# Performance work log

Hardware: AMD Instinct MI355X
Metric: run time of the kernel (lower is better)

The kernel has to match this reference:

```python
import jax, jax.numpy as jnp
import numpy as np

B, N, M, D = 8, 1024, 2048, 1024


def setup_inputs() -> dict:
    key = jax.random.key(0)
    k1, k2, k3 = jax.random.split(key, 3)
    text_features = jax.random.normal(k1, (B, N, D), dtype=jnp.float32)
    audio_features = jax.random.normal(k2, (B, M, D), dtype=jnp.float32)
    sigma = jnp.ones((1,), dtype=jnp.float32)  # learnable bandwidth, initial_sigma=1.0
    # audio lengths in [M//4, M) so no softmax row is fully masked
    audio_lengths = jnp.maximum(
        jax.random.randint(k3, (B,), 0, M), M // 4
    ).astype(jnp.int32)
    return {
        "text_features": text_features,
        "audio_features": audio_features,
        "sigma": sigma,
        "audio_lengths": audio_lengths,
    }


def reference(text_features, audio_features, sigma, audio_lengths):
    b, n, d = text_features.shape
    m = audio_features.shape[1]
    s = jnp.abs(sigma[0]) + 1e-8

    # QK^T / sqrt(d)  -> (B, N, M)
    scores = jnp.einsum("bnd,bmd->bnm", text_features, audio_features) / jnp.sqrt(
        jnp.float32(d)
    )

    # Gaussian relative positional bias: -|i/N - j/M|^2 / (2 sigma^2)
    text_pos = jnp.arange(n, dtype=jnp.float32) / n    # (N,)
    audio_pos = jnp.arange(m, dtype=jnp.float32) / m   # (M,)
    d_rel = jnp.abs(text_pos[:, None] - audio_pos[None, :])  # (N, M)
    scores = scores - d_rel**2 / (2.0 * s * s)

    # mask padded audio positions per batch element
    valid = jnp.arange(m)[None, :] < audio_lengths[:, None]  # (B, M) bool
    scores = jnp.where(valid[:, None, :], scores, -jnp.inf)

    attention_weights = jax.nn.softmax(scores, axis=-1)  # (B, N, M)
    enhanced = jnp.einsum("bnm,bmd->bnd", attention_weights, audio_features)
    return enhanced, attention_weights
```

## Files before the change

kernel.cpp:

```cpp
#include <hip/hip_runtime.h>
#include <hip/hip_bf16.h>

#define BB 8
#define NN 1024
#define MM 2048
#define DD 1024

typedef __attribute__((ext_vector_type(8))) __bf16 bfrag8;
typedef __attribute__((ext_vector_type(4))) float ffrag4;

__device__ __forceinline__ unsigned short f2bf(float f) {
  union { float f; unsigned u; } x; x.f = f;
  unsigned r = x.u + 0x7FFFu + ((x.u >> 16) & 1u);
  return (unsigned short)(r >> 16);
}

__device__ __forceinline__ void gload_lds16(const unsigned short* g, unsigned short* l) {
  __builtin_amdgcn_global_load_lds(
      (const __attribute__((address_space(1))) void*)g,
      (__attribute__((address_space(3))) void*)l, 16, 0, 0);
}

#define SCHED0() __builtin_amdgcn_sched_barrier(0)
#define MFMA16x16x32 __builtin_amdgcn_mfma_f32_16x16x32_bf16

__device__ __forceinline__ void stage_half(const unsigned short* gbase, int ldk,
                                           unsigned short* ldst,
                                           int w, int r0, int slog) {
  const unsigned short* g = gbase + (size_t)(w * 8 + r0) * ldk + slog;
  gload_lds16(g, ldst + w * 512);
  gload_lds16(g + (size_t)64 * ldk, ldst + 4096 + w * 512);
}

#define TSTR 68
__global__ __launch_bounds__(256) void ta_prep(
    const float* __restrict__ Q, const float* __restrict__ V,
    unsigned short* __restrict__ Qbf,
    unsigned short* __restrict__ Kbf, unsigned short* __restrict__ VT,
    float* __restrict__ sums)
{
  __shared__ unsigned short Tls[64 * TSTR];
  const int bid = blockIdx.x;
  const int t = threadIdx.x;

  if (bid < 4096) {
    int tt = bid * 256 + t;
    const float4* src = reinterpret_cast<const float4*>(Q) + tt * 2;
    float4 a = src[0], b = src[1];
    ushort4 lo = { f2bf(a.x), f2bf(a.y), f2bf(a.z), f2bf(a.w) };
    ushort4 hi = { f2bf(b.x), f2bf(b.y), f2bf(b.z), f2bf(b.w) };
    ushort4* dst = reinterpret_cast<ushort4*>(Qbf) + tt * 2;
    dst[0] = lo; dst[1] = hi;
  } else if (bid < 8192) {
    const int id = bid - 4096;
    const int dt = id & 15;
    const int mt = (id >> 4) & 31;
    const int b  = id >> 9;

    const float* Vb = V + (size_t)b * MM * DD + (size_t)(mt * 64) * DD + dt * 64;
#pragma unroll
    for (int it = 0; it < 4; ++it) {
      int slot = t + 256 * it;
      int row  = slot >> 4;
      int c4   = slot & 15;
      float4 a = *reinterpret_cast<const float4*>(Vb + (size_t)row * DD + c4 * 4);
      ushort4 h = { f2bf(a.x), f2bf(a.y), f2bf(a.z), f2bf(a.w) };
      *reinterpret_cast<ushort4*>(&Tls[row * TSTR + c4 * 4]) = h;
    }
    __syncthreads();

    unsigned short* Kb = Kbf + (size_t)b * MM * DD + (size_t)(mt * 64) * DD + dt * 64;
    unsigned short* Vt = VT  + (size_t)b * DD * MM + (size_t)(dt * 64) * MM + mt * 64;
#pragma unroll
    for (int it = 0; it < 4; ++it) {
      int slot = t + 256 * it;
      int row  = slot >> 4;
      int c4   = slot & 15;
      *reinterpret_cast<ushort4*>(Kb + (size_t)row * DD + c4 * 4) =
          *reinterpret_cast<const ushort4*>(&Tls[row * TSTR + c4 * 4]);
      ushort4 tv = { Tls[(c4 * 4 + 0) * TSTR + row],
                     Tls[(c4 * 4 + 1) * TSTR + row],
                     Tls[(c4 * 4 + 2) * TSTR + row],
                     Tls[(c4 * 4 + 3) * TSTR + row] };
      *reinterpret_cast<ushort4*>(Vt + (size_t)row * MM + c4 * 4) = tv;
    }
  } else {
    int tt = (bid - 8192) * 256 + t;
    sums[tt] = 0.0f;
  }
}

__global__ void ta_zero(float* __restrict__ sums) {
  int t = blockIdx.x * 256 + threadIdx.x;
  if (t < BB * NN) sums[t] = 0.0f;
}

__global__ __launch_bounds__(512, 2) void ta_gemm1x(
    const unsigned short* __restrict__ Q,
    const unsigned short* __restrict__ K,
    const float* __restrict__ sigma,
    const int* __restrict__ lens,
    unsigned short* __restrict__ Ebf,
    float* __restrict__ rowsum)
{
  const int lin = blockIdx.x + 8 * (blockIdx.y + 4 * blockIdx.z);
  const int wid = (lin & 7) * 32 + (lin >> 3);
  const int bj = wid & 7, bi = (wid >> 3) & 3, b = wid >> 5;

  const int t = threadIdx.x;
  const int lane = t & 63, w = t >> 6;
  const int wr = w >> 2, wc = w & 3;
  __shared__ unsigned short S[73728];

  const unsigned short* Qb = Q + (size_t)b * NN * DD + (size_t)(bi * 256) * DD;
  const unsigned short* Kb = K + (size_t)b * MM * DD + (size_t)(bj * 256) * DD;

  const int r  = lane & 15, qd = lane >> 4;
  const int r0 = (lane >> 3) & 7;
  const int slog = ((lane & 7) ^ r0) << 3;
  const int cs0 = ((qd)     ^ (r & 7)) << 3;
  const int cs1 = ((4 + qd) ^ (r & 7)) << 3;

  ffrag4 acc[8][4] = {};

  {
    unsigned short* T0 = &S[0];
    stage_half(Qb,                        DD, T0,          w, r0, slog);
    stage_half(Qb + (size_t)128 * DD,     DD, T0 + 8192,   w, r0, slog);
    stage_half(Kb,                        DD, T0 + 16384,  w, r0, slog);
    stage_half(Kb + (size_t)128 * DD,     DD, T0 + 24576,  w, r0, slog);
    unsigned short* T1 = &S[32768];
    stage_half(Qb + 64,                    DD, T1,          w, r0, slog);
    stage_half(Qb + (size_t)128 * DD + 64, DD, T1 + 8192,   w, r0, slog);
    stage_half(Kb + 64,                    DD, T1 + 16384,  w, r0, slog);
    stage_half(Kb + (size_t)128 * DD + 64, DD, T1 + 24576,  w, r0, slog);
    asm volatile("s_waitcnt vmcnt(8)" ::: "memory");
    __builtin_amdgcn_s_barrier();
  }

#pragma unroll 2
  for (int kt = 0; kt < 16; ++kt) {
    const int p = kt & 1;
    unsigned short* Ab = &S[p * 32768 + wr * 8192];
    unsigned short* Bb = &S[p * 32768 + 16384 + (wc >> 1) * 8192];
    const int brb = (wc & 1) * 64;
    bfrag8 af[4][2], bf0[2][2], bf1[2][2];

#pragma unroll
    for (int mi = 0; mi < 4; ++mi) {
      const unsigned short* a = &Ab[(mi * 16 + r) * 64];
      af[mi][0] = *reinterpret_cast<const bfrag8*>(a + cs0);
      af[mi][1] = *reinterpret_cast<const bfrag8*>(a + cs1);
    }
#pragma unroll
    for (int jj = 0; jj < 2; ++jj) {
      const unsigned short* bp = &Bb[(brb + jj * 16 + r) * 64];
      bf0[jj][0] = *reinterpret_cast<const bfrag8*>(bp + cs0);
      bf0[jj][1] = *reinterpret_cast<const bfrag8*>(bp + cs1);
    }
    asm volatile("s_waitcnt lgkmcnt(0)" ::: "memory");
    SCHED0(); __builtin_amdgcn_s_setprio(1);
#pragma unroll
    for (int mi = 0; mi < 4; ++mi)
#pragma unroll
      for (int jj = 0; jj < 2; ++jj) {
        acc[mi][jj] = MFMA16x16x32(af[mi][0], bf0[jj][0], acc[mi][jj], 0, 0, 0);
        acc[mi][jj] = MFMA16x16x32(af[mi][1], bf0[jj][1], acc[mi][jj], 0, 0, 0);
      }
    __builtin_amdgcn_s_setprio(0); SCHED0();

#pragma unroll
    for (int jj = 0; jj < 2; ++jj) {
      const unsigned short* bp = &Bb[(brb + (2 + jj) * 16 + r) * 64];
      bf1[jj][0] = *reinterpret_cast<const bfrag8*>(bp + cs0);
      bf1[jj][1] = *reinterpret_cast<const bfrag8*>(bp + cs1);
    }
    asm volatile("s_waitcnt lgkmcnt(0)" ::: "memory");
    SCHED0(); __builtin_amdgcn_s_barrier();
    __builtin_amdgcn_s_setprio(1);
#pragma unroll
    for (int mi = 0; mi < 4; ++mi)
#pragma unroll
      for (int jj = 0; jj < 2; ++jj) {
        acc[mi][2 + jj] = MFMA16x16x32(af[mi][0], bf1[jj][0], acc[mi][2 + jj], 0, 0, 0);
        acc[mi][2 + jj] = MFMA16x16x32(af[mi][1], bf1[jj][1], acc[mi][2 + jj], 0, 0, 0);
      }
    __builtin_amdgcn_s_setprio(0); SCHED0();

#pragma unroll
    for (int mi = 0; mi < 4; ++mi) {
      const unsigned short* a = &Ab[((mi + 4) * 16 + r) * 64];
      af[mi][0] = *reinterpret_cast<const bfrag8*>(a + cs0);
      af[mi][1] = *reinterpret_cast<const bfrag8*>(a + cs1);
    }
    if (kt + 2 < 16) {
      unsigned short* Dst = &S[p * 32768 + 16384];
      stage_half(Kb + (kt + 2) * 64,                    DD, Dst,        w, r0, slog);
      stage_half(Kb + (size_t)128 * DD + (kt + 2) * 64, DD, Dst + 8192, w, r0, slog);
    }
    asm volatile("s_waitcnt lgkmcnt(0)" ::: "memory");
    SCHED0(); __builtin_amdgcn_s_barrier();
    __builtin_amdgcn_s_setprio(1);
#pragma unroll
    for (int mi = 0; mi < 4; ++mi)
#pragma unroll
      for (int jj = 0; jj < 2; ++jj) {
        acc[4 + mi][2 + jj] = MFMA16x16x32(af[mi][0], bf1[jj][0], acc[4 + mi][2 + jj], 0, 0, 0);
        acc[4 + mi][2 + jj] = MFMA16x16x32(af[mi][1], bf1[jj][1], acc[4 + mi][2 + jj], 0, 0, 0);
      }
    __builtin_amdgcn_s_setprio(0); SCHED0();

    if (kt + 2 < 16) {
      unsigned short* Dst = &S[p * 32768];
      stage_half(Qb + (kt + 2) * 64,                    DD, Dst,        w, r0, slog);
      stage_half(Qb + (size_t)128 * DD + (kt + 2) * 64, DD, Dst + 8192, w, r0, slog);
    }
    SCHED0(); __builtin_amdgcn_s_setprio(1);
#pragma unroll
    for (int mi = 0; mi < 4; ++mi)
#pragma unroll
      for (int jj = 0; jj < 2; ++jj) {
        acc[4 + mi][jj] = MFMA16x16x32(af[mi][0], bf0[jj][0], acc[4 + mi][jj], 0, 0, 0);
        acc[4 + mi][jj] = MFMA16x16x32(af[mi][1], bf0[jj][1], acc[4 + mi][jj], 0, 0, 0);
      }
    __builtin_amdgcn_s_setprio(0); SCHED0();
    if (kt + 2 < 16)      { asm volatile("s_waitcnt vmcnt(8)" ::: "memory"); }
    else if (kt + 1 < 16) { asm volatile("s_waitcnt vmcnt(0)" ::: "memory"); }
    __builtin_amdgcn_s_barrier();
  }

  const float sg = fabsf(sigma[0]) + 1e-8f;
  const float inv2s2 = 1.0f / (2.0f * sg * sg);
  const int len = lens[b];
  unsigned short* Erow = Ebf + (size_t)b * NN * MM;
  float* sums = rowsum + (size_t)b * NN;
  const int ibase = bi * 256 + wr * 128;
  const int jbase = bj * 256 + wc * 64;
  unsigned short* W = &S[w * 9216];

#pragma unroll
  for (int mi = 0; mi < 8; ++mi) {
#pragma unroll
    for (int v = 0; v < 4; ++v) {
      int lrow = mi * 16 + qd * 4 + v;
      int i = ibase + lrow;
      float psum = 0.0f;
#pragma unroll
      for (int nj = 0; nj < 4; ++nj) {
        int j = jbase + nj * 16 + r;
        float e = 0.0f;
        if (j < len) {
          float dr = (float)i * (1.0f / (float)NN) - (float)j * (1.0f / (float)MM);
          float sc = acc[mi][nj][v] * 0.03125f - dr * dr * inv2s2;
          e = __expf(fminf(sc, 30.0f));
        }
        psum += e;
        W[lrow * 72 + nj * 16 + r] = f2bf(e);
      }
      psum += __shfl_xor(psum, 1);
      psum += __shfl_xor(psum, 2);
      psum += __shfl_xor(psum, 4);
      psum += __shfl_xor(psum, 8);
      if (r == 0) atomicAdd(&sums[i], psum);
    }
  }
  asm volatile("s_waitcnt lgkmcnt(0)" ::: "memory");
  const int rrow = lane >> 3, c8 = lane & 7;
#pragma unroll
  for (int pp = 0; pp < 16; ++pp) {
    int row = pp * 8 + rrow;
    uint4 val = *reinterpret_cast<const uint4*>(&W[row * 72 + c8 * 8]);
    *reinterpret_cast<uint4*>(Erow + (size_t)(ibase + row) * MM + jbase + c8 * 8) = val;
  }
}

__global__ __launch_bounds__(512, 2) void ta_gemm2x(
    const unsigned short* __restrict__ E,
    const unsigned short* __restrict__ VT,
    const float* __restrict__ rowsum,
    float* __restrict__ O,
    float* __restrict__ attn)
{
  const int lin = blockIdx.x + 4 * (blockIdx.y + 8 * blockIdx.z);
  const int wid = (lin & 7) * 32 + (lin >> 3);
  const int bd = wid & 3, bi = (wid >> 2) & 7, b = wid >> 5;

  const int t = threadIdx.x;
  const int lane = t & 63, w = t >> 6;
  const int wr = w >> 2, wc = w & 3;
  __shared__ unsigned short S[49152];

  const unsigned short* Eb = E  + (size_t)b * NN * MM + (size_t)(bi * 128) * MM;
  const unsigned short* Vb = VT + (size_t)b * DD * MM + (size_t)(bd * 256) * MM;

  const int r  = lane & 15, qd = lane >> 4;
  const int r0 = (lane >> 3) & 7;
  const int slog = ((lane & 7) ^ r0) << 3;
  const int cs0 = ((qd)     ^ (r & 7)) << 3;
  const int cs1 = ((4 + qd) ^ (r & 7)) << 3;

  ffrag4 acc[4][4] = {};

  const float* rsB = rowsum + (size_t)b * NN;
  const int arow = t >> 2;
  const int lcb  = (t & 3) * 2;
  const int apc0 = (lcb)     ^ (arow & 7);
  const int apc1 = (lcb + 1) ^ (arow & 7);
  const float ainv = 1.0f / fmaxf(rsB[bi * 128 + arow], 1e-30f);
  float* attnRowBase = attn + ((size_t)b * NN + bi * 128 + arow) * MM;

  {
    stage_half(Eb,                        MM, &S[0],     w, r0, slog);
    stage_half(Vb,                        MM, &S[8192],  w, r0, slog);
    stage_half(Vb + (size_t)128 * MM,     MM, &S[16384], w, r0, slog);
    stage_half(Eb + 64,                    MM, &S[24576],         w, r0, slog);
    stage_half(Vb + 64,                    MM, &S[24576 + 8192],  w, r0, slog);
    stage_half(Vb + (size_t)128 * MM + 64, MM, &S[24576 + 16384], w, r0, slog);
    asm volatile("s_waitcnt vmcnt(6)" ::: "memory");
    __builtin_amdgcn_s_barrier();
  }

#pragma unroll 2
  for (int kt = 0; kt < 32; ++kt) {
    const int p = kt & 1;
    unsigned short* Ab = &S[p * 24576];
    unsigned short* Bb = &S[p * 24576 + 8192 + (wc >> 1) * 8192];
    const int arb = wr * 64;
    const int brb = (wc & 1) * 64;
    bfrag8 af[4][2], bf[4][2];
    const bool awin = ((kt >> 3) == bd);
    uint4 av0, av1;

#pragma unroll
    for (int mi = 0; mi < 4; ++mi) {
      const unsigned short* a = &Ab[(arb + mi * 16 + r) * 64];
      af[mi][0] = *reinterpret_cast<const bfrag8*>(a + cs0);
      af[mi][1] = *reinterpret_cast<const bfrag8*>(a + cs1);
    }
#pragma unroll
    for (int nj = 0; nj < 4; ++nj) {
      const unsigned short* bp = &Bb[(brb + nj * 16 + r) * 64];
      bf[nj][0] = *reinterpret_cast<const bfrag8*>(bp + cs0);
      bf[nj][1] = *reinterpret_cast<const bfrag8*>(bp + cs1);
    }
    if (awin) {
      av0 = *reinterpret_cast<const uint4*>(&Ab[arow * 64 + apc0 * 8]);
      av1 = *reinterpret_cast<const uint4*>(&Ab[arow * 64 + apc1 * 8]);
    }

    asm volatile("s_waitcnt lgkmcnt(0)" ::: "memory");
    SCHED0(); __builtin_amdgcn_s_barrier();

    if (awin) {
      float* dst = attnRowBase + kt * 64 + lcb * 8;
      unsigned u[8] = { av0.x, av0.y, av0.z, av0.w, av1.x, av1.y, av1.z, av1.w };
      float o[16];
#pragma unroll
      for (int k2 = 0; k2 < 8; ++k2) {
        union { unsigned u; float f; } lo, hi;
        lo.u = u[k2] << 16; hi.u = u[k2] & 0xFFFF0000u;
        o[2 * k2]     = lo.f * ainv;
        o[2 * k2 + 1] = hi.f * ainv;
      }
      float4* d4 = reinterpret_cast<float4*>(dst);
      float4 f0 = { o[0],  o[1],  o[2],  o[3]  };
      float4 f1 = { o[4],  o[5],  o[6],  o[7]  };
      float4 f2 = { o[8],  o[9],  o[10], o[11] };
      float4 f3 = { o[12], o[13], o[14], o[15] };
      d4[0] = f0; d4[1] = f1; d4[2] = f2; d4[3] = f3;
    }
    SCHED0();

    __builtin_amdgcn_s_setprio(1);
#pragma unroll
    for (int mi = 0; mi < 2; ++mi)
#pragma unroll
      for (int nj = 0; nj < 4; ++nj) {
        acc[mi][nj] = MFMA16x16x32(af[mi][0], bf[nj][0], acc[mi][nj], 0, 0, 0);
        acc[mi][nj] = MFMA16x16x32(af[mi][1], bf[nj][1], acc[mi][nj], 0, 0, 0);
      }
    __builtin_amdgcn_s_setprio(0); SCHED0();

    if (kt + 2 < 32) {
      unsigned short* Dst = &S[p * 24576];
      stage_half(Eb + (kt + 2) * 64,                    MM, Dst,         w, r0, slog);
      stage_half(Vb + (kt + 2) * 64,                    MM, Dst + 8192,  w, r0, slog);
      stage_half(Vb + (size_t)128 * MM + (kt + 2) * 64, MM, Dst + 16384, w, r0, slog);
    }

    SCHED0(); __builtin_amdgcn_s_setprio(1);
#pragma unroll
    for (int mi = 2; mi < 4; ++mi)
#pragma unroll
      for (int nj = 0; nj < 4; ++nj) {
        acc[mi][nj] = MFMA16x16x32(af[mi][0], bf[nj][0], acc[mi][nj], 0, 0, 0);
        acc[mi][nj] = MFMA16x16x32(af[mi][1], bf[nj][1], acc[mi][nj], 0, 0, 0);
      }
    __builtin_amdgcn_s_setprio(0); SCHED0();

    if (kt + 2 < 32)      { asm volatile("s_waitcnt vmcnt(6)" ::: "memory"); }
    else if (kt + 1 < 32) { asm volatile("s_waitcnt vmcnt(0)" ::: "memory"); }
    __builtin_amdgcn_s_barrier();
  }

  float* Ob = O + (size_t)b * NN * DD;
  const int ibase = bi * 128 + wr * 64;
  const int dbase = bd * 256 + wc * 64;
#pragma unroll
  for (int mi = 0; mi < 4; ++mi) {
#pragma unroll
    for (int v = 0; v < 4; ++v) {
      int i = ibase + mi * 16 + qd * 4 + v;
      float inv = 1.0f / fmaxf(rsB[i], 1e-30f);
#pragma unroll
      for (int nj = 0; nj < 4; ++nj) {
        int d = dbase + nj * 16 + r;
        Ob[(size_t)i * DD + d] = acc[mi][nj][v] * inv;
      }
    }
  }
}

#define LDA 40
__global__ __launch_bounds__(256) void tb_gemm1e(
    const float* __restrict__ Q, const float* __restrict__ K,
    const float* __restrict__ sigma, const int* __restrict__ lens,
    float* __restrict__ attn, float* __restrict__ rowsum)
{
  const int bj = blockIdx.x, bi = blockIdx.y, b = blockIdx.z;
  const int t = threadIdx.x;
  const int lane = t & 63;
  const int w = t >> 6;
  const int wi = w >> 1, wj = w & 1;
  __shared__ unsigned short Als[128 * LDA];
  __shared__ unsigned short Bls[128 * LDA];
  const float* Qb = Q + (size_t)b * NN * DD + (size_t)(bi * 128) * DD;
  const float* Kb = K + (size_t)b * MM * DD + (size_t)(bj * 128) * DD;
  ffrag4 acc[4][4] = {};
  const int r = lane & 15;
  const int koff = (lane >> 4) * 8;
  for (int k0 = 0; k0 < DD; k0 += 32) {
#pragma unroll
    for (int it = 0; it < 4; ++it) {
      int slot = t + 256 * it;
      int row = slot >> 3, c4 = slot & 7;
      float4 qa = *reinterpret_cast<const float4*>(Qb + (size_t)row * DD + k0 + c4 * 4);
      float4 ka = *reinterpret_cast<const float4*>(Kb + (size_t)row * DD + k0 + c4 * 4);
      ushort4 qh = { f2bf(qa.x), f2bf(qa.y), f2bf(qa.z), f2bf(qa.w) };
      ushort4 kh = { f2bf(ka.x), f2bf(ka.y), f2bf(ka.z), f2bf(ka.w) };
      *reinterpret_cast<ushort4*>(&Als[row * LDA + c4 * 4]) = qh;
      *reinterpret_cast<ushort4*>(&Bls[row * LDA + c4 * 4]) = kh;
    }
    __syncthreads();
    bfrag8 af[4], bf[4];
#pragma unroll
    for (int ti = 0; ti < 4; ++ti)
      af[ti] = *reinterpret_cast<const bfrag8*>(&Als[(wi * 64 + ti * 16 + r) * LDA + koff]);
#pragma unroll
    for (int tj = 0; tj < 4; ++tj)
      bf[tj] = *reinterpret_cast<const bfrag8*>(&Bls[(wj * 64 + tj * 16 + r) * LDA + koff]);
#pragma unroll
    for (int ti = 0; ti < 4; ++ti)
#pragma unroll
      for (int tj = 0; tj < 4; ++tj)
        acc[ti][tj] = MFMA16x16x32(af[ti], bf[tj], acc[ti][tj], 0, 0, 0);
    __syncthreads();
  }
  const float s = fabsf(sigma[0]) + 1e-8f;
  const float inv2s2 = 1.0f / (2.0f * s * s);
  const int len = lens[b];
  float* Prow = attn + (size_t)b * NN * MM;
  float* sums = rowsum + (size_t)b * NN;
  const int ibase = bi * 128 + wi * 64;
  const int jbase = bj * 128 + wj * 64;
  const int quad = lane >> 4;
#pragma unroll
  for (int ti = 0; ti < 4; ++ti) {
#pragma unroll
    for (int v = 0; v < 4; ++v) {
      int i = ibase + ti * 16 + quad * 4 + v;
      float psum = 0.0f;
#pragma unroll
      for (int tj = 0; tj < 4; ++tj) {
        int j = jbase + tj * 16 + r;
        float e = 0.0f;
        if (j < len) {
          float dr = (float)i * (1.0f / (float)NN) - (float)j * (1.0f / (float)MM);
          float sc = acc[ti][tj][v] * 0.03125f - dr * dr * inv2s2;
          e = __expf(fminf(sc, 30.0f));
        }
        psum += e;
        Prow[(size_t)i * MM + j] = e;
      }
      psum += __shfl_xor(psum, 1);
      psum += __shfl_xor(psum, 2);
      psum += __shfl_xor(psum, 4);
      psum += __shfl_xor(psum, 8);
      if (r == 0) atomicAdd(&sums[i], psum);
    }
  }
}

__global__ __launch_bounds__(256) void tb_norm(float* __restrict__ attn,
                                               const float* __restrict__ sums) {
  int t = blockIdx.x * 256 + threadIdx.x;
  int row = t >> 9;
  const float inv = 1.0f / fmaxf(sums[row], 1e-30f);
  float4* p = reinterpret_cast<float4*>(attn) + t;
  float4 x = *p;
  x.x *= inv; x.y *= inv; x.z *= inv; x.w *= inv;
  *p = x;
}

__global__ __launch_bounds__(256) void tb_gemm2(
    const float* __restrict__ P, const float* __restrict__ V, float* __restrict__ O)
{
  const int bd = blockIdx.x, bi = blockIdx.y, b = blockIdx.z;
  const int t = threadIdx.x;
  const int lane = t & 63;
  const int w = t >> 6;
  const int wi = w >> 1, wj = w & 1;
  __shared__ unsigned short Pls[128 * LDA];
  __shared__ unsigned short Vls[128 * LDA];
  const float* Pb = P + (size_t)b * NN * MM + (size_t)(bi * 128) * MM;
  const float* Vb = V + (size_t)b * MM * DD + bd * 128;
  ffrag4 acc[4][4] = {};
  const int r = lane & 15;
  const int koff = (lane >> 4) * 8;
  const int vd = t & 127;
  const int vmb = (t >> 7) * 16;
  for (int k0 = 0; k0 < MM; k0 += 32) {
#pragma unroll
    for (int it = 0; it < 4; ++it) {
      int slot = t + 256 * it;
      int row = slot >> 3, c4 = slot & 7;
      float4 pa = *reinterpret_cast<const float4*>(Pb + (size_t)row * MM + k0 + c4 * 4);
      ushort4 ph = { f2bf(pa.x), f2bf(pa.y), f2bf(pa.z), f2bf(pa.w) };
      *reinterpret_cast<ushort4*>(&Pls[row * LDA + c4 * 4]) = ph;
    }
    union { unsigned short h[16]; uint4 q[2]; } hv;
#pragma unroll
    for (int i = 0; i < 16; ++i)
      hv.h[i] = f2bf(Vb[(size_t)(k0 + vmb + i) * DD + vd]);
    *reinterpret_cast<uint4*>(&Vls[vd * LDA + vmb]) = hv.q[0];
    *reinterpret_cast<uint4*>(&Vls[vd * LDA + vmb + 8]) = hv.q[1];
    __syncthreads();
    bfrag8 af[4], bf[4];
#pragma unroll
    for (int ti = 0; ti < 4; ++ti)
      af[ti] = *reinterpret_cast<const bfrag8*>(&Pls[(wi * 64 + ti * 16 + r) * LDA + koff]);
#pragma unroll
    for (int tj = 0; tj < 4; ++tj)
      bf[tj] = *reinterpret_cast<const bfrag8*>(&Vls[(wj * 64 + tj * 16 + r) * LDA + koff]);
#pragma unroll
    for (int ti = 0; ti < 4; ++ti)
#pragma unroll
      for (int tj = 0; tj < 4; ++tj)
        acc[ti][tj] = MFMA16x16x32(af[ti], bf[tj], acc[ti][tj], 0, 0, 0);
    __syncthreads();
  }
  float* Ob = O + (size_t)b * NN * DD;
  const int ibase = bi * 128 + wi * 64;
  const int dbase = bd * 128 + wj * 64;
#pragma unroll
  for (int ti = 0; ti < 4; ++ti) {
#pragma unroll
    for (int tj = 0; tj < 4; ++tj) {
      int d = dbase + tj * 16 + r;
#pragma unroll
      for (int v = 0; v < 4; ++v) {
        int i = ibase + ti * 16 + (lane >> 4) * 4 + v;
        Ob[(size_t)i * DD + d] = acc[ti][tj][v];
      }
    }
  }
}

extern "C" void kernel_launch(void* const* d_in, const int* in_sizes, int n_in,
                              void* d_out, int out_size, void* d_ws, size_t ws_size,
                              hipStream_t stream) {
  const float* text  = (const float*)d_in[0];
  const float* audio = (const float*)d_in[1];
  const float* sigma = (const float*)d_in[2];
  const int*   lens  = (const int*)d_in[3];

  float* out = (float*)d_out;
  float* enhanced = out;
  float* attn = out + (size_t)BB * NN * DD;

  const size_t QBF  = (size_t)BB * NN * DD * 2;
  const size_t KBF  = (size_t)BB * MM * DD * 2;
  const size_t VTB  = (size_t)BB * DD * MM * 2;
  const size_t EBF  = (size_t)BB * NN * MM * 2;
  const size_t offQ = 65536;
  const size_t offK = offQ + QBF;
  const size_t offV = offK + KBF;
  const size_t offE = offV + VTB;
  const size_t need = offE + EBF;

  float* rowsum = (float*)d_ws;

  if (ws_size >= need) {
    unsigned short* Qbf = (unsigned short*)((char*)d_ws + offQ);
    unsigned short* Kbf = (unsigned short*)((char*)d_ws + offK);
    unsigned short* VT  = (unsigned short*)((char*)d_ws + offV);
    unsigned short* Ebf = (unsigned short*)((char*)d_ws + offE);

    ta_prep<<<dim3(8224), 256, 0, stream>>>(text, audio, Qbf, Kbf, VT, rowsum);
    ta_gemm1x<<<dim3(MM / 256, NN / 256, BB), 512, 0, stream>>>(Qbf, Kbf, sigma, lens, Ebf, rowsum);
    ta_gemm2x<<<dim3(DD / 256, NN / 128, BB), 512, 0, stream>>>(Ebf, VT, rowsum, enhanced, attn);
  } else {
    ta_zero<<<dim3((BB * NN + 255) / 256), 256, 0, stream>>>(rowsum);
    tb_gemm1e<<<dim3(MM / 128, NN / 128, BB), 256, 0, stream>>>(text, audio, sigma, lens, attn, rowsum);
    tb_norm<<<dim3(BB * NN * MM / 4 / 256), 256, 0, stream>>>(attn, rowsum);
    tb_gemm2<<<dim3(DD / 128, NN / 128, BB), 256, 0, stream>>>(attn, audio, enhanced);
  }
}
```

Before: 265.7 us.

## Use deeper multi-buffered LDS pipelines with one barrier per K-step in both GEMMs

The QK^T kernel moves from a 2-stage, 64-wide K tile pipeline with several barriers per step to a 4-stage ring of 32-wide K tiles. Each step issues the prefetch three tiles ahead and then runs all 32 MFMAs behind a single barrier. The PV kernel moves from double buffering to a 3-buffer ring. Its prefetch is issued at the top of the step and the mid-step barrier is removed, so loads overlap compute and synchronisation drops. The cost is more LDS in the PV kernel, which may lower occupancy, plus new swizzle and index logic that could cause bank conflicts.

```diff
diff --git a/kernel.cpp b/kernel.cpp
--- a/kernel.cpp
+++ b/kernel.cpp
@@ -30,6 +30,14 @@
   const unsigned short* g = gbase + (size_t)(w * 8 + r0) * ldk + slog;
   gload_lds16(g, ldst + w * 512);
   gload_lds16(g + (size_t)64 * ldk, ldst + 4096 + w * 512);
+}
+
+__device__ __forceinline__ void stage_op32(const unsigned short* gbase, int ldk,
+                                           unsigned short* L,
+                                           int w, int srow, int sloc) {
+  const unsigned short* g0 = gbase + (size_t)(w * 32 + srow) * ldk + sloc;
+  gload_lds16(g0, L + w * 1024);
+  gload_lds16(g0 + (size_t)16 * ldk, L + w * 1024 + 512);
 }
 
 #define TSTR 68
@@ -116,118 +124,59 @@
   const unsigned short* Kb = K + (size_t)b * MM * DD + (size_t)(bj * 256) * DD;
 
   const int r  = lane & 15, qd = lane >> 4;
-  const int r0 = (lane >> 3) & 7;
-  const int slog = ((lane & 7) ^ r0) << 3;
-  const int cs0 = ((qd)     ^ (r & 7)) << 3;
-  const int cs1 = ((4 + qd) ^ (r & 7)) << 3;
+  const int srow = lane >> 2;
+  const int sloc = ((lane & 3) ^ (srow & 3)) << 3;
+  const int fco  = (qd ^ (r & 3)) << 3;
 
   ffrag4 acc[8][4] = {};
 
   {
-    unsigned short* T0 = &S[0];
-    stage_half(Qb,                        DD, T0,          w, r0, slog);
-    stage_half(Qb + (size_t)128 * DD,     DD, T0 + 8192,   w, r0, slog);
-    stage_half(Kb,                        DD, T0 + 16384,  w, r0, slog);
-    stage_half(Kb + (size_t)128 * DD,     DD, T0 + 24576,  w, r0, slog);
-    unsigned short* T1 = &S[32768];
-    stage_half(Qb + 64,                    DD, T1,          w, r0, slog);
-    stage_half(Qb + (size_t)128 * DD + 64, DD, T1 + 8192,   w, r0, slog);
-    stage_half(Kb + 64,                    DD, T1 + 16384,  w, r0, slog);
-    stage_half(Kb + (size_t)128 * DD + 64, DD, T1 + 24576,  w, r0, slog);
+    stage_op32(Qb,      DD, &S[0],            w, srow, sloc);
+    stage_op32(Kb,      DD, &S[8192],         w, srow, sloc);
+    stage_op32(Qb + 32, DD, &S[16384],        w, srow, sloc);
+    stage_op32(Kb + 32, DD, &S[16384 + 8192], w, srow, sloc);
+    stage_op32(Qb + 64, DD, &S[32768],        w, srow, sloc);
+    stage_op32(Kb + 64, DD, &S[32768 + 8192], w, srow, sloc);
     asm volatile("s_waitcnt vmcnt(8)" ::: "memory");
     __builtin_amdgcn_s_barrier();
   }
 
-#pragma unroll 2
-  for (int kt = 0; kt < 16; ++kt) {
-    const int p = kt & 1;
-    unsigned short* Ab = &S[p * 32768 + wr * 8192];
-    unsigned short* Bb = &S[p * 32768 + 16384 + (wc >> 1) * 8192];
-    const int brb = (wc & 1) * 64;
-    bfrag8 af[4][2], bf0[2][2], bf1[2][2];
-
-#pragma unroll
-    for (int mi = 0; mi < 4; ++mi) {
-      const unsigned short* a = &Ab[(mi * 16 + r) * 64];
-      af[mi][0] = *reinterpret_cast<const bfrag8*>(a + cs0);
-      af[mi][1] = *reinterpret_cast<const bfrag8*>(a + cs1);
-    }
-#pragma unroll
-    for (int jj = 0; jj < 2; ++jj) {
-      const unsigned short* bp = &Bb[(brb + jj * 16 + r) * 64];
-      bf0[jj][0] = *reinterpret_cast<const bfrag8*>(bp + cs0);
-      bf0[jj][1] = *reinterpret_cast<const bfrag8*>(bp + cs1);
-    }
+#pragma unroll 4
+  for (int kt = 0; kt < 32; ++kt) {
+    unsigned short* Buf = &S[(kt & 3) * 16384];
+
+    if (kt + 3 < 32) {
+      unsigned short* D = &S[((kt + 3) & 3) * 16384];
+      const int k0 = (kt + 3) * 32;
+      stage_op32(Qb + k0, DD, D,        w, srow, sloc);
+      stage_op32(Kb + k0, DD, D + 8192, w, srow, sloc);
+    }
+
+    bfrag8 af[8], bf[4];
+    const unsigned short* Ar = Buf + (wr * 128 + r) * 32 + fco;
+    const unsigned short* Br = Buf + 8192 + (wc * 64 + r) * 32 + fco;
+#pragma unroll
+    for (int mi = 0; mi < 8; ++mi)
+      af[mi] = *reinterpret_cast<const bfrag8*>(Ar + mi * 512);
+#pragma unroll
+    for (int nj = 0; nj < 4; ++nj)
+      bf[nj] = *reinterpret_cast<const bfrag8*>(Br + nj * 512);
+
     asm volatile("s_waitcnt lgkmcnt(0)" ::: "memory");
     SCHED0(); __builtin_amdgcn_s_setprio(1);
 #pragma unroll
-    for (int mi = 0; mi < 4; ++mi)
-#pragma unroll
-      for (int jj = 0; jj < 2; ++jj) {
-        acc[mi][jj] = MFMA16x16x32(af[mi][0], bf0[jj][0], acc[mi][jj], 0, 0, 0);
-        acc[mi][jj] = MFMA16x16x32(af[mi][1], bf0[jj][1], acc[mi][jj], 0, 0, 0);
-      }
+    for (int mi = 0; mi < 8; ++mi)
+#pragma unroll
+      for (int nj = 0; nj < 4; ++nj)
+        acc[mi][nj] = MFMA16x16x32(af[mi], bf[nj], acc[mi][nj], 0, 0, 0);
     __builtin_amdgcn_s_setprio(0); SCHED0();
 
-#pragma unroll
-    for (int jj = 0; jj < 2; ++jj) {
-      const unsigned short* bp = &Bb[(brb + (2 + jj) * 16 + r) * 64];
-      bf1[jj][0] = *reinterpret_cast<const bfrag8*>(bp + cs0);
-      bf1[jj][1] = *reinterpret_cast<const bfrag8*>(bp + cs1);
-    }
-    asm volatile("s_waitcnt lgkmcnt(0)" ::: "memory");
-    SCHED0(); __builtin_amdgcn_s_barrier();
-    __builtin_amdgcn_s_setprio(1);
-#pragma unroll
-    for (int mi = 0; mi < 4; ++mi)
-#pragma unroll
-      for (int jj = 0; jj < 2; ++jj) {
-        acc[mi][2 + jj] = MFMA16x16x32(af[mi][0], bf1[jj][0], acc[mi][2 + jj], 0, 0, 0);
-        acc[mi][2 + jj] = MFMA16x16x32(af[mi][1], bf1[jj][1], acc[mi][2 + jj], 0, 0, 0);
-      }
-    __builtin_amdgcn_s_setprio(0); SCHED0();
-
-#pragma unroll
-    for (int mi = 0; mi < 4; ++mi) {
-      const unsigned short* a = &Ab[((mi + 4) * 16 + r) * 64];
-      af[mi][0] = *reinterpret_cast<const bfrag8*>(a + cs0);
-      af[mi][1] = *reinterpret_cast<const bfrag8*>(a + cs1);
-    }
-    if (kt + 2 < 16) {
-      unsigned short* Dst = &S[p * 32768 + 16384];
-      stage_half(Kb + (kt + 2) * 64,                    DD, Dst,        w, r0, slog);
-      stage_half(Kb + (size_t)128 * DD + (kt + 2) * 64, DD, Dst + 8192, w, r0, slog);
-    }
-    asm volatile("s_waitcnt lgkmcnt(0)" ::: "memory");
-    SCHED0(); __builtin_amdgcn_s_barrier();
-    __builtin_amdgcn_s_setprio(1);
-#pragma unroll
-    for (int mi = 0; mi < 4; ++mi)
-#pragma unroll
-      for (int jj = 0; jj < 2; ++jj) {
-        acc[4 + mi][2 + jj] = MFMA16x16x32(af[mi][0], bf1[jj][0], acc[4 + mi][2 + jj], 0, 0, 0);
-        acc[4 + mi][2 + jj] = MFMA16x16x32(af[mi][1], bf1[jj][1], acc[4 + mi][2 + jj], 0, 0, 0);
-      }
-    __builtin_amdgcn_s_setprio(0); SCHED0();
-
-    if (kt + 2 < 16) {
-      unsigned short* Dst = &S[p * 32768];
-      stage_half(Qb + (kt + 2) * 64,                    DD, Dst,        w, r0, slog);
-      stage_half(Qb + (size_t)128 * DD + (kt + 2) * 64, DD, Dst + 8192, w, r0, slog);
-    }
-    SCHED0(); __builtin_amdgcn_s_setprio(1);
-#pragma unroll
-    for (int mi = 0; mi < 4; ++mi)
-#pragma unroll
-      for (int jj = 0; jj < 2; ++jj) {
-        acc[4 + mi][jj] = MFMA16x16x32(af[mi][0], bf0[jj][0], acc[4 + mi][jj], 0, 0, 0);
-        acc[4 + mi][jj] = MFMA16x16x32(af[mi][1], bf0[jj][1], acc[4 + mi][jj], 0, 0, 0);
-      }
-    __builtin_amdgcn_s_setprio(0); SCHED0();
-    if (kt + 2 < 16)      { asm volatile("s_waitcnt vmcnt(8)" ::: "memory"); }
-    else if (kt + 1 < 16) { asm volatile("s_waitcnt vmcnt(0)" ::: "memory"); }
-    __builtin_amdgcn_s_barrier();
-  }
+    if (kt < 29)       { asm volatile("s_waitcnt vmcnt(8)" ::: "memory"); }
+    else if (kt == 29) { asm volatile("s_waitcnt vmcnt(4)" ::: "memory"); }
+    else if (kt == 30) { asm volatile("s_waitcnt vmcnt(0)" ::: "memory"); }
+    if (kt < 31) __builtin_amdgcn_s_barrier();
+  }
+  __syncthreads();
 
   const float sg = fabsf(sigma[0]) + 1e-8f;
   const float inv2s2 = 1.0f / (2.0f * sg * sg);
@@ -288,7 +237,7 @@
   const int t = threadIdx.x;
   const int lane = t & 63, w = t >> 6;
   const int wr = w >> 2, wc = w & 3;
-  __shared__ unsigned short S[49152];
+  __shared__ unsigned short S[73728];
 
   const unsigned short* Eb = E  + (size_t)b * NN * MM + (size_t)(bi * 128) * MM;
   const unsigned short* Vb = VT + (size_t)b * DD * MM + (size_t)(bd * 256) * MM;
@@ -320,17 +269,24 @@
     __builtin_amdgcn_s_barrier();
   }
 
-#pragma unroll 2
+  int cur = 0;
   for (int kt = 0; kt < 32; ++kt) {
-    const int p = kt & 1;
-    unsigned short* Ab = &S[p * 24576];
-    unsigned short* Bb = &S[p * 24576 + 8192 + (wc >> 1) * 8192];
+    unsigned short* Tb = &S[cur * 24576];
+    unsigned short* Ab = Tb;
+    unsigned short* Bb = Tb + 8192 + (wc >> 1) * 8192;
     const int arb = wr * 64;
     const int brb = (wc & 1) * 64;
+
+    if (kt + 2 < 32) {
+      int nb = cur + 2; if (nb >= 3) nb -= 3;
+      unsigned short* D = &S[nb * 24576];
+      const int k0 = (kt + 2) * 64;
+      stage_half(Eb + k0,                    MM, D,         w, r0, slog);
+      stage_half(Vb + k0,                    MM, D + 8192,  w, r0, slog);
+      stage_half(Vb + (size_t)128 * MM + k0, MM, D + 16384, w, r0, slog);
+    }
+
     bfrag8 af[4][2], bf[4][2];
-    const bool awin = ((kt >> 3) == bd);
-    uint4 av0, av1;
-
 #pragma unroll
     for (int mi = 0; mi < 4; ++mi) {
       const unsigned short* a = &Ab[(arb + mi * 16 + r) * 64];
@@ -343,15 +299,10 @@
       bf[nj][0] = *reinterpret_cast<const bfrag8*>(bp + cs0);
       bf[nj][1] = *reinterpret_cast<const bfrag8*>(bp + cs1);
     }
-    if (awin) {
-      av0 = *reinterpret_cast<const uint4*>(&Ab[arow * 64 + apc0 * 8]);
-      av1 = *reinterpret_cast<const uint4*>(&Ab[arow * 64 + apc1 * 8]);
-    }
-
-    asm volatile("s_waitcnt lgkmcnt(0)" ::: "memory");
-    SCHED0(); __builtin_amdgcn_s_barrier();
-
-    if (awin) {
+
+    if ((kt >> 3) == bd) {
+      uint4 av0 = *reinterpret_cast<const uint4*>(&Ab[arow * 64 + apc0 * 8]);
+      uint4 av1 = *reinterpret_cast<const uint4*>(&Ab[arow * 64 + apc1 * 8]);
       float* dst = attnRowBase + kt * 64 + lcb * 8;
       unsigned u[8] = { av0.x, av0.y, av0.z, av0.w, av1.x, av1.y, av1.z, av1.w };
       float o[16];
@@ -369,11 +320,11 @@
       float4 f3 = { o[12], o[13], o[14], o[15] };
       d4[0] = f0; d4[1] = f1; d4[2] = f2; d4[3] = f3;
     }
-    SCHED0();
-
-    __builtin_amdgcn_s_setprio(1);
-#pragma unroll
-    for (int mi = 0; mi < 2; ++mi)
+
+    asm volatile("s_waitcnt lgkmcnt(0)" ::: "memory");
+    SCHED0(); __builtin_amdgcn_s_setprio(1);
+#pragma unroll
+    for (int mi = 0; mi < 4; ++mi)
 #pragma unroll
       for (int nj = 0; nj < 4; ++nj) {
         acc[mi][nj] = MFMA16x16x32(af[mi][0], bf[nj][0], acc[mi][nj], 0, 0, 0);
@@ -381,26 +332,10 @@
       }
     __builtin_amdgcn_s_setprio(0); SCHED0();
 
-    if (kt + 2 < 32) {
-      unsigned short* Dst = &S[p * 24576];
-      stage_half(Eb + (kt + 2) * 64,                    MM, Dst,         w, r0, slog);
-      stage_half(Vb + (kt + 2) * 64,                    MM, Dst + 8192,  w, r0, slog);
-      stage_half(Vb + (size_t)128 * MM + (kt + 2) * 64, MM, Dst + 16384, w, r0, slog);
-    }
-
-    SCHED0(); __builtin_amdgcn_s_setprio(1);
-#pragma unroll
-    for (int mi = 2; mi < 4; ++mi)
-#pragma unroll
-      for (int nj = 0; nj < 4; ++nj) {
-        acc[mi][nj] = MFMA16x16x32(af[mi][0], bf[nj][0], acc[mi][nj], 0, 0, 0);
-        acc[mi][nj] = MFMA16x16x32(af[mi][1], bf[nj][1], acc[mi][nj], 0, 0, 0);
-      }
-    __builtin_amdgcn_s_setprio(0); SCHED0();
-
-    if (kt + 2 < 32)      { asm volatile("s_waitcnt vmcnt(6)" ::: "memory"); }
-    else if (kt + 1 < 32) { asm volatile("s_waitcnt vmcnt(0)" ::: "memory"); }
-    __builtin_amdgcn_s_barrier();
+    if (kt < 30)       { asm volatile("s_waitcnt vmcnt(6)" ::: "memory"); }
+    else if (kt == 30) { asm volatile("s_waitcnt vmcnt(0)" ::: "memory"); }
+    if (kt < 31) __builtin_amdgcn_s_barrier();
+    cur += 1; if (cur == 3) cur = 0;
   }
 
   float* Ob = O + (size_t)b * NN * DD;
```

Result: no change. 269.9 us (+1.6%).
